# Kernel optimization log

Measured on AMD Instinct MI355X. Metric: run time of the kernel, lower is better.

The kernel has to match this reference:

```python
import jax, jax.numpy as jnp
import numpy as np

NUM_AUDIOS = 64
NODES_PER = 800
N = NUM_AUDIOS * NODES_PER  # 51200
DEG = 8
E = N * DEG  # 409600
IN_C, HID, OUT, HEADS = 512, 256, 256, 2
NEG_SLOPE = 0.2  # PyG GATConv default


def setup_inputs() -> dict:
    key = jax.random.key(0)
    ks = jax.random.split(key, 12)
    x = jax.random.normal(ks[0], (N, IN_C), jnp.float32)
    # edges strictly inside each audio's node block (PyG batching: no cross-graph edges)
    src_l = jax.random.randint(ks[1], (NUM_AUDIOS, NODES_PER * DEG), 0, NODES_PER)
    dst_l = jax.random.randint(ks[2], (NUM_AUDIOS, NODES_PER * DEG), 0, NODES_PER)
    off = (jnp.arange(NUM_AUDIOS) * NODES_PER)[:, None]
    edge_index = jnp.stack([(src_l + off).reshape(-1), (dst_l + off).reshape(-1)]).astype(jnp.int32)
    batch = jnp.repeat(jnp.arange(NUM_AUDIOS), NODES_PER).astype(jnp.int32)

    def gl(k, shape, fan):
        return (jax.random.normal(k, shape, jnp.float32) / np.sqrt(fan)).astype(jnp.float32)

    W1 = gl(ks[3], (IN_C, HEADS * HID), IN_C)
    a_s1 = gl(ks[4], (HEADS, HID), HID)
    a_d1 = gl(ks[5], (HEADS, HID), HID)
    b1 = jnp.zeros((HID,), jnp.float32)
    W2 = gl(ks[6], (HID, HEADS * OUT), HID)
    a_s2 = gl(ks[7], (HEADS, OUT), OUT)
    a_d2 = gl(ks[8], (HEADS, OUT), OUT)
    b2 = jnp.zeros((OUT,), jnp.float32)
    w_att = gl(ks[9], (OUT, 1), OUT)
    b_att = jnp.zeros((1,), jnp.float32)
    w_cls = gl(ks[10], (OUT, 2), OUT)
    b_cls = jnp.zeros((2,), jnp.float32)
    return dict(x=x, edge_index=edge_index, batch=batch,
                W1=W1, a_s1=a_s1, a_d1=a_d1, b1=b1,
                W2=W2, a_s2=a_s2, a_d2=a_d2, b2=b2,
                w_att=w_att, b_att=b_att, w_cls=w_cls, b_cls=b_cls)


def _gat(x, src, dst, W, a_s, a_d, b):
    """PyG GATConv(heads=H, concat=False): linear -> per-edge LeakyReLU scores ->
    softmax over incoming edges (with self-loops) -> scatter-sum -> head-mean + bias."""
    n = x.shape[0]
    H, C = a_s.shape
    h = (x @ W).reshape(n, H, C)                      # [N,H,C]
    al_s = jnp.einsum('nhc,hc->nh', h, a_s)           # [N,H]
    al_d = jnp.einsum('nhc,hc->nh', h, a_d)
    loop = jnp.arange(n, dtype=src.dtype)             # add self-loops (default)
    s = jnp.concatenate([src, loop])
    d = jnp.concatenate([dst, loop])
    e = jax.nn.leaky_relu(al_s[s] + al_d[d], NEG_SLOPE)  # [E+N,H]
    mx = jax.ops.segment_max(e, d, num_segments=n)
    w = jnp.exp(e - mx[d])
    den = jax.ops.segment_sum(w, d, num_segments=n)
    alpha = w / den[d]
    out = jax.ops.segment_sum(h[s] * alpha[:, :, None], d, num_segments=n)  # [N,H,C]
    return out.mean(axis=1) + b


def reference(x, edge_index, batch, W1, a_s1, a_d1, b1, W2, a_s2, a_d2, b2,
              w_att, b_att, w_cls, b_cls):
    src, dst = edge_index[0], edge_index[1]
    h = jax.nn.relu(_gat(x, src, dst, W1, a_s1, a_d1, b1))
    node_emb = _gat(h, src, dst, W2, a_s2, a_d2, b2)
    # per-audio temporal attention: softmax over nodes within each audio segment.
    # (edges never cross audio boundaries, so the per-subgraph GAT re-run in the
    #  original Python loop equals the full-graph GAT restricted to each segment.)
    logits = node_emb @ w_att + b_att                 # [N,1]
    mx = jax.ops.segment_max(logits, batch, num_segments=NUM_AUDIOS)
    w = jnp.exp(logits - mx[batch])
    den = jax.ops.segment_sum(w, batch, num_segments=NUM_AUDIOS)
    attn = w / den[batch]                             # [N,1]
    attended = jax.ops.segment_sum(attn * node_emb, batch, num_segments=NUM_AUDIOS)  # [A,OUT]
    audio_result = attended @ w_cls + b_cls           # [A,2]
    return node_emb, audio_result
```

## Files before the change

### kernel.cpp

```cpp
#include <hip/hip_runtime.h>
#include <cstdint>
#include <cstddef>

#define NUM_AUDIOS 64
#define NODES_PER  800
#define NN         51200
#define EE         409600

typedef __attribute__((ext_vector_type(8))) unsigned short ushort8;
typedef __attribute__((ext_vector_type(4))) unsigned short ushort4v;
typedef __attribute__((ext_vector_type(8))) __bf16 bf16x8;
typedef __attribute__((ext_vector_type(4))) float f32x4;

__device__ __forceinline__ float b2f(unsigned short h) {
  return __uint_as_float(((unsigned)h) << 16);
}
__device__ __forceinline__ unsigned short f2b(float f) {
  unsigned u = __float_as_uint(f);
  u += 0x7fffu + ((u >> 16) & 1u);
  return (unsigned short)(u >> 16);
}
__device__ __forceinline__ float lrelu(float v) { return v > 0.f ? v : 0.2f * v; }

#define P_AS1 0
#define P_AD1 512
#define P_B1  1024
#define P_AS2 1536
#define P_AD2 2048
#define P_B2  2560
#define P_WATT 3072
#define P_BATT 3328
#define P_WCLS 3336
#define P_BCLS 3848

#define ZERO_F4 132096
#define ZERO_BLOCKS 516

__global__ __launch_bounds__(256) void prolog0_k(float4* __restrict__ zbase,
                                                 const unsigned short* __restrict__ x,
                                                 int* __restrict__ flag) {
  const int i = blockIdx.x * 256 + threadIdx.x;
  if (i < ZERO_F4) zbase[i] = (float4){0.f, 0.f, 0.f, 0.f};
  if (blockIdx.x == 0) {
    __shared__ int s;
    if (threadIdx.x == 0) s = 0;
    __syncthreads();
    int big = 0;
    for (int k = threadIdx.x; k < 4096; k += 256) {
      const float v = b2f(x[k]);
      if (!(__builtin_fabsf(v) <= 1e4f)) big = 1;
    }
    if (big) atomicOr(&s, 1);
    __syncthreads();
    if (threadIdx.x == 0) *flag = s;
  }
}

#define PB_PAR  10
#define PB_T1   (PB_PAR + 1024)
#define PB_T2   (PB_T1 + 512)
#define PB_HIST (PB_T2 + 1600)

__global__ __launch_bounds__(256) void prep_k(
    const void* __restrict__ W1, unsigned short* __restrict__ W1T,
    const void* __restrict__ W2, unsigned short* __restrict__ W2T,
    const void* p0, const void* p1, const void* p2, const void* p3, const void* p4,
    const void* p5, const void* p6, const void* p7, const void* p8, const void* p9,
    unsigned short* __restrict__ params,
    const int* __restrict__ dst, int* __restrict__ counts,
    const int* __restrict__ flagp) {
  const int b = blockIdx.x, tid = threadIdx.x;
  const int f = *flagp;
  if (b < PB_PAR) {
    const void* srcs[10] = {p0, p1, p2, p3, p4, p5, p6, p7, p8, p9};
    const int offs[10] = {P_AS1, P_AD1, P_B1, P_AS2, P_AD2, P_B2, P_WATT, P_BATT, P_WCLS, P_BCLS};
    const int lens[10] = {512, 512, 256, 512, 512, 256, 256, 1, 512, 2};
    const int s = b;
    for (int i = tid; i < lens[s]; i += 256)
      params[offs[s] + i] = f ? f2b(((const float*)srcs[s])[i])
                              : ((const unsigned short*)srcs[s])[i];
  } else if (b < PB_T1) {
    const int idx = (b - PB_PAR) * 256 + tid;
    const int n = idx >> 9, k = idx & 511;
    W1T[idx] = f ? f2b(((const float*)W1)[(size_t)k * 512 + n])
                 : ((const unsigned short*)W1)[(size_t)k * 512 + n];
  } else if (b < PB_T2) {
    const int idx = (b - PB_T1) * 256 + tid;
    const int n = idx >> 8, k = idx & 255;
    W2T[idx] = f ? f2b(((const float*)W2)[(size_t)k * 512 + n])
                 : ((const unsigned short*)W2)[(size_t)k * 512 + n];
  } else {
    const int e = (b - PB_T2) * 256 + tid;
    atomicAdd(&counts[dst[e]], 1);
  }
}

__global__ __launch_bounds__(256) void rowptr_k(const int* __restrict__ counts, int* __restrict__ row_ptr) {
  __shared__ int sh[800];
  __shared__ int pre[200];
  const int a = blockIdx.x, t = threadIdx.x;
  for (int i = t; i < 800; i += 256) sh[i] = counts[a * 800 + i];
  __syncthreads();
  if (t < 200) pre[t] = sh[t * 4] + sh[t * 4 + 1] + sh[t * 4 + 2] + sh[t * 4 + 3];
  __syncthreads();
  if (t == 0) {
    int run = 0;
    for (int i = 0; i < 200; ++i) { const int v = pre[i]; pre[i] = run; run += v; }
  }
  __syncthreads();
  if (t < 200) {
    int b = a * 6400 + pre[t];
#pragma unroll
    for (int j = 0; j < 4; ++j) { row_ptr[a * 800 + t * 4 + j] = b; b += sh[t * 4 + j]; }
  }
}

__global__ __launch_bounds__(256) void scatter_k(const int* __restrict__ src, const int* __restrict__ dst,
                                                 const int* __restrict__ row_ptr, int* __restrict__ cursor,
                                                 int* __restrict__ ssrc) {
  const int e = blockIdx.x * 256 + threadIdx.x;
  const int d = dst[e];
  const int p = atomicAdd(&cursor[d], 1);
  ssrc[row_ptr[d] + p] = src[e];
}

__device__ __forceinline__ void mfma_tile(const unsigned short* As, const unsigned short* Bs,
                                          int wm, int wn, int row, int quad, f32x4 acc[4][4]) {
  bf16x8 af[4], bq[4];
  const int pa = (quad ^ (row & 3)) * 8;
#pragma unroll
  for (int i = 0; i < 4; ++i) {
    af[i] = *(const bf16x8*)&As[(wm * 64 + i * 16 + row) * 32 + pa];
    bq[i] = *(const bf16x8*)&Bs[(wn * 64 + i * 16 + row) * 32 + pa];
  }
#pragma unroll
  for (int i = 0; i < 4; ++i)
#pragma unroll
    for (int j = 0; j < 4; ++j)
      acc[i][j] = __builtin_amdgcn_mfma_f32_16x16x32_bf16(af[i], bq[j], acc[i][j], 0, 0, 0);
}

__global__ __launch_bounds__(256) void gemm_bt(const void* __restrict__ Araw,
                                               const unsigned short* __restrict__ BT,
                                               unsigned short* __restrict__ C,
                                               int K, int Nn,
                                               const unsigned short* __restrict__ a_s,
                                               const unsigned short* __restrict__ a_d,
                                               float* __restrict__ al_s,
                                               float* __restrict__ al_d,
                                               const int* __restrict__ aflag) {
  __shared__ unsigned short smem[16384];
  const int tid = threadIdx.x;
  const int wave = tid >> 6, lane = tid & 63;
  const int bid = blockIdx.x;
  const int g = bid & 7, bt = bid >> 3;
  const int m0 = (g * 50 + (bt >> 2)) * 128;
  const int n0 = (bt & 3) * 128;
  const int wm = wave >> 1, wn = wave & 1;
  const int row = lane & 15, quad = lane >> 4;
  f32x4 acc[4][4];
#pragma unroll
  for (int i = 0; i < 4; ++i)
#pragma unroll
    for (int j = 0; j < 4; ++j) acc[i][j] = (f32x4){0.f, 0.f, 0.f, 0.f};

  const bool a_is_f32 = (aflag != nullptr) && (*aflag != 0);
  const unsigned short* A16 = (const unsigned short*)Araw;
  const float* A32 = (const float*)Araw;
  const int srow0 = tid >> 2;
  const int kph = tid & 3;

  if (!a_is_f32) {
    const int nk = K >> 5;
    auto stage = [&](int buf, int k0) {
      unsigned short* Asb = smem + buf * 8192;
      unsigned short* Bsb = Asb + 4096;
#pragma unroll
      for (int r = 0; r < 2; ++r) {
        const int arow = r * 64 + srow0;
        const int kc = ((kph ^ (arow & 3)) * 8);
        __builtin_amdgcn_global_load_lds(
            (const __attribute__((address_space(1))) void*)(A16 + (size_t)(m0 + arow) * K + k0 + kc),
            (__attribute__((address_space(3))) void*)(Asb + (r * 256 + wave * 64) * 8),
            16, 0, 0);
        __builtin_amdgcn_global_load_lds(
            (const __attribute__((address_space(1))) void*)(BT + (size_t)(n0 + arow) * K + k0 + kc),
            (__attribute__((address_space(3))) void*)(Bsb + (r * 256 + wave * 64) * 8),
            16, 0, 0);
      }
    };
    stage(0, 0);
    for (int t = 0; t < nk; ++t) {
      const int cur = t & 1;
      if (t + 1 < nk) {
        stage(cur ^ 1, (t + 1) << 5);
        asm volatile("s_waitcnt vmcnt(4)" ::: "memory");
      } else {
        asm volatile("s_waitcnt vmcnt(0)" ::: "memory");
      }
      __builtin_amdgcn_sched_barrier(0);
      __builtin_amdgcn_s_barrier();
      __builtin_amdgcn_sched_barrier(0);
      mfma_tile(smem + cur * 8192, smem + cur * 8192 + 4096, wm, wn, row, quad, acc);
      __builtin_amdgcn_sched_barrier(0);
      __builtin_amdgcn_s_barrier();
    }
  } else {
    unsigned short* As = smem;
    unsigned short* Bs = smem + 4096;
    for (int k0 = 0; k0 < K; k0 += 32) {
      ushort8 pk[2];
#pragma unroll
      for (int r = 0; r < 2; ++r) {
        const int arow = r * 64 + srow0;
        const int kc = ((kph ^ (arow & 3)) * 8);
        const float* p = A32 + (size_t)(m0 + arow) * K + k0 + kc;
        const float4 f0 = *(const float4*)p;
        const float4 f1 = *(const float4*)(p + 4);
        pk[r][0] = f2b(f0.x); pk[r][1] = f2b(f0.y); pk[r][2] = f2b(f0.z); pk[r][3] = f2b(f0.w);
        pk[r][4] = f2b(f1.x); pk[r][5] = f2b(f1.y); pk[r][6] = f2b(f1.z); pk[r][7] = f2b(f1.w);
      }
      __syncthreads();
#pragma unroll
      for (int r = 0; r < 2; ++r) {
        const int arow = r * 64 + srow0;
        const int kc = ((kph ^ (arow & 3)) * 8);
        __builtin_amdgcn_global_load_lds(
            (const __attribute__((address_space(1))) void*)(BT + (size_t)(n0 + arow) * K + k0 + kc),
            (__attribute__((address_space(3))) void*)(Bs + (size_t)(r * 256 + wave * 64) * 8),
            16, 0, 0);
        *(ushort8*)&As[(size_t)(r * 256 + tid) * 8] = pk[r];
      }
      __syncthreads();
      mfma_tile(As, Bs, wm, wn, row, quad, acc);
    }
  }

  const int col = lane & 15;
  __syncthreads();
  {
#pragma unroll
    for (int i = 0; i < 4; ++i)
#pragma unroll
      for (int jj = 0; jj < 4; ++jj) {
#pragma unroll
        for (int r = 0; r < 4; ++r) {
          const int rl = wm * 64 + i * 16 + quad * 4 + r;
          const int pc = (wn * 4 + jj) ^ quad;
          smem[rl * 128 + pc * 16 + col] = f2b(acc[i][jj][r]);
        }
      }
  }
  __syncthreads();
  {
    const int rloc = tid >> 4;
    const int c8 = (tid & 15) * 8;
    const int lc = c8 >> 4;
    const int coff = c8 & 15;
#pragma unroll
    for (int s = 0; s < 8; ++s) {
      const int rl = s * 16 + rloc;
      const int q = (rl >> 2) & 3;
      const ushort8 v = *(const ushort8*)&smem[rl * 128 + (lc ^ q) * 16 + coff];
      *(ushort8*)&C[(size_t)(m0 + rl) * Nn + n0 + c8] = v;
    }
  }

  {
    const int head = (n0 + wn * 64) >> 8;
    float as4[4], ad4[4];
#pragma unroll
    for (int j = 0; j < 4; ++j) {
      const int gn = n0 + wn * 64 + j * 16 + col;
      as4[j] = b2f(a_s[gn]);
      ad4[j] = b2f(a_d[gn]);
    }
#pragma unroll
    for (int i = 0; i < 4; ++i)
#pragma unroll
      for (int r = 0; r < 4; ++r) {
        float ps = 0.f, pd = 0.f;
#pragma unroll
        for (int j = 0; j < 4; ++j) { ps += acc[i][j][r] * as4[j]; pd += acc[i][j][r] * ad4[j]; }
#pragma unroll
        for (int off = 1; off < 16; off <<= 1) {
          ps += __shfl_xor(ps, off);
          pd += __shfl_xor(pd, off);
        }
        if (col == 0) {
          const int gm = m0 + wm * 64 + i * 16 + quad * 4 + r;
          atomicAdd(&al_s[gm * 2 + head], ps);
          atomicAdd(&al_d[gm * 2 + head], pd);
        }
      }
  }
}

__global__ __launch_bounds__(256) void agg_k(const unsigned short* __restrict__ h,
                                             const float* __restrict__ al_s, const float* __restrict__ al_d,
                                             const int* __restrict__ row_ptr, const int* __restrict__ counts,
                                             const int* __restrict__ ssrc, const unsigned short* __restrict__ bias,
                                             unsigned short* __restrict__ out, int do_relu,
                                             void* __restrict__ out2, const int* __restrict__ flagp,
                                             const unsigned short* __restrict__ watt,
                                             float* __restrict__ lg) {
  const int wave = threadIdx.x >> 6, lane = threadIdx.x & 63;
  const int b = blockIdx.x;
  const int g = b & 7, r = b >> 3;
  const int a = g + 8 * (r / 200);
  const int chunk = r % 200;
  const int n = a * 800 + chunk * 4 + wave;
  const int head = lane >> 5;
  const int hl = lane & 31;
  const int hsel = lane & 32;
  const int deg = counts[n];
  const int base = row_ptr[n];
  const float ald = al_d[n * 2 + head];
  const float self_e = lrelu(al_s[n * 2 + head] + ald);

  float m = -1e30f;
  for (int i = hl; i < deg; i += 32) {
    const int s = ssrc[base + i];
    m = fmaxf(m, al_s[s * 2 + head]);
  }
#pragma unroll
  for (int off = 1; off < 32; off <<= 1) m = fmaxf(m, __shfl_xor(m, off));
  const float mx = fmaxf(lrelu(m + ald), self_e);

  const float w_self = __expf(self_e - mx);
  float acc[8];
  {
    const ushort8 hv = *(const ushort8*)&h[(unsigned)(n * 512 + lane * 8)];
#pragma unroll
    for (int j = 0; j < 8; ++j) acc[j] = w_self * b2f(hv[j]);
  }
  float dpart = 0.f;
  for (int t0 = 0; t0 < deg; t0 += 32) {
    const int cnt = min(32, deg - t0);
    int s = 0; float w = 0.f;
    if (hl < cnt) {
      s = ssrc[base + t0 + hl];
      w = __expf(lrelu(al_s[s * 2 + head] + ald) - mx);
      dpart += w;
    }
    for (int i = 0; i < cnt; ++i) {
      const float wb = __shfl(w, hsel + i);
      const int sb = __shfl(s, hsel + i);
      const ushort8 hv = *(const ushort8*)&h[(unsigned)(sb * 512 + lane * 8)];
#pragma unroll
      for (int j = 0; j < 8; ++j) acc[j] += wb * b2f(hv[j]);
    }
  }
#pragma unroll
  for (int off = 1; off < 32; off <<= 1) dpart += __shfl_xor(dpart, off);
  const float inv = 1.f / (w_self + dpart);

  const int c0 = hl * 8;
  ushort8 res;
  float ov[8];
#pragma unroll
  for (int j = 0; j < 8; ++j) {
    const float mine = acc[j] * inv;
    const float other = __shfl_xor(mine, 32);
    float o = (mine + other) * 0.5f + b2f(bias[c0 + j]);
    if (do_relu) o = fmaxf(o, 0.f);
    ov[j] = o;
    res[j] = f2b(o);
  }
  if (lane < 32) {
    *(ushort8*)&out[(unsigned)(n * 256 + c0)] = res;
    if (out2) {
      if (*flagp) {
        float4* p = (float4*)((float*)out2 + (size_t)n * 256 + c0);
        p[0] = (float4){ov[0], ov[1], ov[2], ov[3]};
        p[1] = (float4){ov[4], ov[5], ov[6], ov[7]};
      } else {
        *(ushort8*)((unsigned short*)out2 + (size_t)n * 256 + c0) = res;
      }
    }
    if (lg) {
      const ushort8 wv = *(const ushort8*)&watt[c0];
      float d = 0.f;
#pragma unroll
      for (int j = 0; j < 8; ++j) d += ov[j] * b2f(wv[j]);
#pragma unroll
      for (int off = 1; off < 32; off <<= 1) d += __shfl_xor(d, off);
      if (hl == 0) lg[n] = d + b2f(watt[256]);
    }
  }
}

__global__ __launch_bounds__(256) void stats_k(const float* __restrict__ lg,
                                               float* __restrict__ mxv, float* __restrict__ invv) {
  __shared__ float red[256];
  const int a = blockIdx.x, t = threadIdx.x;
  float m = -1e30f;
  for (int i = t; i < 800; i += 256) m = fmaxf(m, lg[a * 800 + i]);
  red[t] = m; __syncthreads();
  for (int s = 128; s >= 1; s >>= 1) { if (t < s) red[t] = fmaxf(red[t], red[t + s]); __syncthreads(); }
  const float mx = red[0];
  __syncthreads();
  float sum = 0.f;
  for (int i = t; i < 800; i += 256) sum += __expf(lg[a * 800 + i] - mx);
  red[t] = sum; __syncthreads();
  for (int s = 128; s >= 1; s >>= 1) { if (t < s) red[t] += red[t + s]; __syncthreads(); }
  if (t == 0) { mxv[a] = mx; invv[a] = 1.f / red[0]; }
}

__global__ __launch_bounds__(256) void attended_k(const unsigned short* __restrict__ emb,
                                                  const float* __restrict__ lg,
                                                  const float* __restrict__ mxv,
                                                  const float* __restrict__ invv,
                                                  float* __restrict__ attended) {
  const int b = blockIdx.x;
  const int a = b >> 3, chunk = b & 7;
  const int t = threadIdx.x;
  __shared__ float ws[100];
  const int i0 = chunk * 100;
  const float mx = mxv[a], inv = invv[a];
  if (t < 100) ws[t] = __expf(lg[a * 800 + i0 + t] - mx) * inv;
  __syncthreads();
  float acc = 0.f;
  const unsigned short* base = emb + ((size_t)(a * 800 + i0)) * 256 + t;
#pragma unroll 4
  for (int j = 0; j < 100; ++j) acc += ws[j] * b2f(base[(size_t)j * 256]);
  atomicAdd(&attended[a * 256 + t], acc);
}

__global__ __launch_bounds__(256) void cls_k(const float* __restrict__ attended,
                                             const unsigned short* __restrict__ params,
                                             void* __restrict__ out, const int* __restrict__ flag) {
  __shared__ float red[256];
  const int a = blockIdx.x, t = threadIdx.x;
  const float v = attended[a * 256 + t];
  const float p0 = v * b2f(params[P_WCLS + t * 2]);
  const float p1 = v * b2f(params[P_WCLS + t * 2 + 1]);
  red[t] = p0; __syncthreads();
  for (int s = 128; s >= 1; s >>= 1) { if (t < s) red[t] += red[t + s]; __syncthreads(); }
  const float r0 = red[0];
  __syncthreads();
  red[t] = p1; __syncthreads();
  for (int s = 128; s >= 1; s >>= 1) { if (t < s) red[t] += red[t + s]; __syncthreads(); }
  const float r1 = red[0];
  if (t == 0) {
    const float o0 = r0 + b2f(params[P_BCLS]);
    const float o1 = r1 + b2f(params[P_BCLS + 1]);
    if (*flag) {
      ((float*)out)[(size_t)NN * 256 + a * 2]     = o0;
      ((float*)out)[(size_t)NN * 256 + a * 2 + 1] = o1;
    } else {
      ((unsigned short*)out)[(size_t)NN * 256 + a * 2]     = f2b(o0);
      ((unsigned short*)out)[(size_t)NN * 256 + a * 2 + 1] = f2b(o1);
    }
  }
}

extern "C" void kernel_launch(void* const* d_in, const int* in_sizes, int n_in,
                              void* d_out, int out_size, void* d_ws, size_t ws_size,
                              hipStream_t stream) {
  (void)in_sizes; (void)n_in; (void)out_size; (void)ws_size;
  const void* x_raw  = d_in[0];
  const int*  eidx   = (const int*)d_in[1];
  const int* src = eidx;
  const int* dst = eidx + EE;

  char* ws = (char*)d_ws;
  size_t off = 0;
  auto alloc = [&](size_t bytes) -> void* {
    void* p = ws + off;
    off += (bytes + 255) & ~(size_t)255;
    return p;
  };
  int* flag              = (int*)alloc(256);
  unsigned short* params = (unsigned short*)alloc(4096 * 2);
  unsigned short* W1T    = (unsigned short*)alloc((size_t)512 * 512 * 2);
  unsigned short* W2T    = (unsigned short*)alloc((size_t)512 * 256 * 2);
  unsigned short* scr    = (unsigned short*)alloc((size_t)NN * 512 * 2);
  unsigned short* hbig   = (unsigned short*)alloc((size_t)NN * 512 * 2);
  int*   counts   = (int*)alloc((size_t)NN * 4);
  int*   cursor   = (int*)alloc((size_t)NN * 4);
  float* attended = (float*)alloc((size_t)NUM_AUDIOS * 256 * 4);
  float* al_s1    = (float*)alloc((size_t)NN * 2 * 4);
  float* al_d1    = (float*)alloc((size_t)NN * 2 * 4);
  float* al_s2    = (float*)alloc((size_t)NN * 2 * 4);
  float* al_d2    = (float*)alloc((size_t)NN * 2 * 4);
  int*   rowp   = (int*)alloc((size_t)NN * 4);
  int*   ssrc   = (int*)alloc((size_t)EE * 4);
  float* lg     = (float*)alloc((size_t)NN * 4);
  float* mxv    = (float*)alloc(NUM_AUDIOS * 4);
  float* invv   = (float*)alloc(NUM_AUDIOS * 4);
  unsigned short* hrel  = scr;
  unsigned short* emb16 = scr + (size_t)NN * 256;

  prolog0_k<<<dim3(ZERO_BLOCKS), 256, 0, stream>>>((float4*)counts,
                                                   (const unsigned short*)x_raw, flag);

  prep_k<<<dim3(PB_HIST), 256, 0, stream>>>(
      d_in[3], W1T, d_in[7], W2T,
      d_in[4], d_in[5], d_in[6], d_in[8], d_in[9],
      d_in[10], d_in[11], d_in[12], d_in[13], d_in[14],
      params, dst, counts, flag);

  rowptr_k<<<dim3(NUM_AUDIOS), 256, 0, stream>>>(counts, rowp);
  scatter_k<<<dim3(EE / 256), 256, 0, stream>>>(src, dst, rowp, cursor, ssrc);

  gemm_bt<<<dim3(1600), 256, 0, stream>>>(x_raw, W1T, hbig, 512, 512,
                                          params + P_AS1, params + P_AD1, al_s1, al_d1, flag);
  agg_k<<<dim3(NN / 4), 256, 0, stream>>>(hbig, al_s1, al_d1, rowp, counts, ssrc,
                                          params + P_B1, hrel, 1, nullptr, flag,
                                          params + P_WATT, nullptr);

  gemm_bt<<<dim3(1600), 256, 0, stream>>>(hrel, W2T, hbig, 256, 512,
                                          params + P_AS2, params + P_AD2, al_s2, al_d2, nullptr);
  agg_k<<<dim3(NN / 4), 256, 0, stream>>>(hbig, al_s2, al_d2, rowp, counts, ssrc,
                                          params + P_B2, emb16, 0, d_out, flag,
                                          params + P_WATT, lg);

  stats_k<<<dim3(NUM_AUDIOS), 256, 0, stream>>>(lg, mxv, invv);
  attended_k<<<dim3(NUM_AUDIOS * 8), 256, 0, stream>>>(emb16, lg, mxv, invv, attended);
  cls_k<<<dim3(NUM_AUDIOS), 256, 0, stream>>>(attended, params, d_out, flag);
}
```

Before: 449.2 us.

## Enlarge GEMM tile to 256x256 with 512 threads and reduce attention logits in LDS

The projection GEMM moves from 128x128 tiles with 256 threads to 256x256 tiles with 512 threads (8 waves, each 128x64), so each block covers a full head of columns. This raises operand reuse per LDS load and cuts the grid from 1600 to 400 blocks. The per-row attention logits are now summed across waves in shared memory and written with plain stores instead of global atomics, which works because one block owns a whole head. The tradeoff is more accumulator registers per thread, double the LDS use, fewer blocks to spread over the CUs, and an epilogue that writes the output in two halves.

```diff
diff --git a/kernel.cpp b/kernel.cpp
--- a/kernel.cpp
+++ b/kernel.cpp
@@ -8,7 +8,6 @@
 #define EE         409600
 
 typedef __attribute__((ext_vector_type(8))) unsigned short ushort8;
-typedef __attribute__((ext_vector_type(4))) unsigned short ushort4v;
 typedef __attribute__((ext_vector_type(8))) __bf16 bf16x8;
 typedef __attribute__((ext_vector_type(4))) float f32x4;
 
@@ -124,43 +123,46 @@
   ssrc[row_ptr[d] + p] = src[e];
 }
 
-__device__ __forceinline__ void mfma_tile(const unsigned short* As, const unsigned short* Bs,
-                                          int wm, int wn, int row, int quad, f32x4 acc[4][4]) {
-  bf16x8 af[4], bq[4];
+__device__ __forceinline__ void mfma_tile256(const unsigned short* As, const unsigned short* Bs,
+                                             int wm, int wn, int row, int quad, f32x4 acc[8][4]) {
+  bf16x8 af[8], bq[4];
   const int pa = (quad ^ (row & 3)) * 8;
 #pragma unroll
-  for (int i = 0; i < 4; ++i) {
-    af[i] = *(const bf16x8*)&As[(wm * 64 + i * 16 + row) * 32 + pa];
-    bq[i] = *(const bf16x8*)&Bs[(wn * 64 + i * 16 + row) * 32 + pa];
-  }
-#pragma unroll
-  for (int i = 0; i < 4; ++i)
+  for (int i = 0; i < 8; ++i)
+    af[i] = *(const bf16x8*)&As[(wm * 128 + i * 16 + row) * 32 + pa];
+#pragma unroll
+  for (int j = 0; j < 4; ++j)
+    bq[j] = *(const bf16x8*)&Bs[(wn * 64 + j * 16 + row) * 32 + pa];
+#pragma unroll
+  for (int i = 0; i < 8; ++i)
 #pragma unroll
     for (int j = 0; j < 4; ++j)
       acc[i][j] = __builtin_amdgcn_mfma_f32_16x16x32_bf16(af[i], bq[j], acc[i][j], 0, 0, 0);
 }
 
-__global__ __launch_bounds__(256) void gemm_bt(const void* __restrict__ Araw,
-                                               const unsigned short* __restrict__ BT,
-                                               unsigned short* __restrict__ C,
-                                               int K, int Nn,
-                                               const unsigned short* __restrict__ a_s,
-                                               const unsigned short* __restrict__ a_d,
-                                               float* __restrict__ al_s,
-                                               float* __restrict__ al_d,
-                                               const int* __restrict__ aflag) {
-  __shared__ unsigned short smem[16384];
+__global__ __launch_bounds__(512, 2) void gemm_bt(const void* __restrict__ Araw,
+                                                  const unsigned short* __restrict__ BT,
+                                                  unsigned short* __restrict__ C,
+                                                  int K, int Nn,
+                                                  const unsigned short* __restrict__ a_s,
+                                                  const unsigned short* __restrict__ a_d,
+                                                  float* __restrict__ al_s,
+                                                  float* __restrict__ al_d,
+                                                  const int* __restrict__ aflag) {
+  __shared__ unsigned short smem[32768];
   const int tid = threadIdx.x;
   const int wave = tid >> 6, lane = tid & 63;
   const int bid = blockIdx.x;
   const int g = bid & 7, bt = bid >> 3;
-  const int m0 = (g * 50 + (bt >> 2)) * 128;
-  const int n0 = (bt & 3) * 128;
-  const int wm = wave >> 1, wn = wave & 1;
+  const int mt = bt >> 1, nt = bt & 1;
+  const int m0 = (g * 25 + mt) * 256;
+  const int n0 = nt * 256;
+  const int wm = wave >> 2, wn = wave & 3;
   const int row = lane & 15, quad = lane >> 4;
-  f32x4 acc[4][4];
-#pragma unroll
-  for (int i = 0; i < 4; ++i)
+  const int col = lane & 15;
+  f32x4 acc[8][4];
+#pragma unroll
+  for (int i = 0; i < 8; ++i)
 #pragma unroll
     for (int j = 0; j < 4; ++j) acc[i][j] = (f32x4){0.f, 0.f, 0.f, 0.f};
 
@@ -173,19 +175,19 @@
   if (!a_is_f32) {
     const int nk = K >> 5;
     auto stage = [&](int buf, int k0) {
-      unsigned short* Asb = smem + buf * 8192;
-      unsigned short* Bsb = Asb + 4096;
-#pragma unroll
-      for (int r = 0; r < 2; ++r) {
-        const int arow = r * 64 + srow0;
+      unsigned short* Asb = smem + buf * 16384;
+      unsigned short* Bsb = Asb + 8192;
+#pragma unroll
+      for (int p = 0; p < 2; ++p) {
+        const int arow = p * 128 + srow0;
         const int kc = ((kph ^ (arow & 3)) * 8);
         __builtin_amdgcn_global_load_lds(
             (const __attribute__((address_space(1))) void*)(A16 + (size_t)(m0 + arow) * K + k0 + kc),
-            (__attribute__((address_space(3))) void*)(Asb + (r * 256 + wave * 64) * 8),
+            (__attribute__((address_space(3))) void*)(Asb + (p * 512 + tid) * 8),
             16, 0, 0);
         __builtin_amdgcn_global_load_lds(
             (const __attribute__((address_space(1))) void*)(BT + (size_t)(n0 + arow) * K + k0 + kc),
-            (__attribute__((address_space(3))) void*)(Bsb + (r * 256 + wave * 64) * 8),
+            (__attribute__((address_space(3))) void*)(Bsb + (p * 512 + tid) * 8),
             16, 0, 0);
       }
     };
@@ -201,73 +203,45 @@
       __builtin_amdgcn_sched_barrier(0);
       __builtin_amdgcn_s_barrier();
       __builtin_amdgcn_sched_barrier(0);
-      mfma_tile(smem + cur * 8192, smem + cur * 8192 + 4096, wm, wn, row, quad, acc);
+      mfma_tile256(smem + cur * 16384, smem + cur * 16384 + 8192, wm, wn, row, quad, acc);
       __builtin_amdgcn_sched_barrier(0);
       __builtin_amdgcn_s_barrier();
     }
   } else {
     unsigned short* As = smem;
-    unsigned short* Bs = smem + 4096;
+    unsigned short* Bs = smem + 8192;
     for (int k0 = 0; k0 < K; k0 += 32) {
       ushort8 pk[2];
 #pragma unroll
-      for (int r = 0; r < 2; ++r) {
-        const int arow = r * 64 + srow0;
+      for (int p = 0; p < 2; ++p) {
+        const int arow = p * 128 + srow0;
         const int kc = ((kph ^ (arow & 3)) * 8);
-        const float* p = A32 + (size_t)(m0 + arow) * K + k0 + kc;
-        const float4 f0 = *(const float4*)p;
-        const float4 f1 = *(const float4*)(p + 4);
-        pk[r][0] = f2b(f0.x); pk[r][1] = f2b(f0.y); pk[r][2] = f2b(f0.z); pk[r][3] = f2b(f0.w);
-        pk[r][4] = f2b(f1.x); pk[r][5] = f2b(f1.y); pk[r][6] = f2b(f1.z); pk[r][7] = f2b(f1.w);
+        const float* ap = A32 + (size_t)(m0 + arow) * K + k0 + kc;
+        const float4 f0 = *(const float4*)ap;
+        const float4 f1 = *(const float4*)(ap + 4);
+        pk[p][0] = f2b(f0.x); pk[p][1] = f2b(f0.y); pk[p][2] = f2b(f0.z); pk[p][3] = f2b(f0.w);
+        pk[p][4] = f2b(f1.x); pk[p][5] = f2b(f1.y); pk[p][6] = f2b(f1.z); pk[p][7] = f2b(f1.w);
       }
       __syncthreads();
 #pragma unroll
-      for (int r = 0; r < 2; ++r) {
-        const int arow = r * 64 + srow0;
+      for (int p = 0; p < 2; ++p) {
+        const int arow = p * 128 + srow0;
         const int kc = ((kph ^ (arow & 3)) * 8);
         __builtin_amdgcn_global_load_lds(
             (const __attribute__((address_space(1))) void*)(BT + (size_t)(n0 + arow) * K + k0 + kc),
-            (__attribute__((address_space(3))) void*)(Bs + (size_t)(r * 256 + wave * 64) * 8),
+            (__attribute__((address_space(3))) void*)(Bs + (size_t)(p * 512 + tid) * 8),
             16, 0, 0);
-        *(ushort8*)&As[(size_t)(r * 256 + tid) * 8] = pk[r];
+        *(ushort8*)&As[(size_t)(p * 512 + tid) * 8] = pk[p];
       }
       __syncthreads();
-      mfma_tile(As, Bs, wm, wn, row, quad, acc);
-    }
-  }
-
-  const int col = lane & 15;
-  __syncthreads();
+      mfma_tile256(As, Bs, wm, wn, row, quad, acc);
+    }
+  }
+
+  __syncthreads();
+
   {
-#pragma unroll
-    for (int i = 0; i < 4; ++i)
-#pragma unroll
-      for (int jj = 0; jj < 4; ++jj) {
-#pragma unroll
-        for (int r = 0; r < 4; ++r) {
-          const int rl = wm * 64 + i * 16 + quad * 4 + r;
-          const int pc = (wn * 4 + jj) ^ quad;
-          smem[rl * 128 + pc * 16 + col] = f2b(acc[i][jj][r]);
-        }
-      }
-  }
-  __syncthreads();
-  {
-    const int rloc = tid >> 4;
-    const int c8 = (tid & 15) * 8;
-    const int lc = c8 >> 4;
-    const int coff = c8 & 15;
-#pragma unroll
-    for (int s = 0; s < 8; ++s) {
-      const int rl = s * 16 + rloc;
-      const int q = (rl >> 2) & 3;
-      const ushort8 v = *(const ushort8*)&smem[rl * 128 + (lc ^ q) * 16 + coff];
-      *(ushort8*)&C[(size_t)(m0 + rl) * Nn + n0 + c8] = v;
-    }
-  }
-
-  {
-    const int head = (n0 + wn * 64) >> 8;
+    float* alb = (float*)smem;
     float as4[4], ad4[4];
 #pragma unroll
     for (int j = 0; j < 4; ++j) {
@@ -276,7 +250,7 @@
       ad4[j] = b2f(a_d[gn]);
     }
 #pragma unroll
-    for (int i = 0; i < 4; ++i)
+    for (int i = 0; i < 8; ++i)
 #pragma unroll
       for (int r = 0; r < 4; ++r) {
         float ps = 0.f, pd = 0.f;
@@ -288,11 +262,49 @@
           pd += __shfl_xor(pd, off);
         }
         if (col == 0) {
-          const int gm = m0 + wm * 64 + i * 16 + quad * 4 + r;
-          atomicAdd(&al_s[gm * 2 + head], ps);
-          atomicAdd(&al_d[gm * 2 + head], pd);
+          const int rr = wm * 128 + i * 16 + quad * 4 + r;
+          alb[(0 * 4 + wn) * 256 + rr] = ps;
+          alb[(1 * 4 + wn) * 256 + rr] = pd;
         }
       }
+  }
+  __syncthreads();
+  {
+    const float* alb = (const float*)smem;
+    const int rr = tid >> 1, kind = tid & 1;
+    float s = 0.f;
+#pragma unroll
+    for (int w = 0; w < 4; ++w) s += alb[(kind * 4 + w) * 256 + rr];
+    float* dstp = kind ? al_d : al_s;
+    dstp[(size_t)(m0 + rr) * 2 + nt] = s;
+  }
+  __syncthreads();
+
+#pragma unroll
+  for (int half = 0; half < 2; ++half) {
+    if (wm == half) {
+#pragma unroll
+      for (int i = 0; i < 8; ++i)
+#pragma unroll
+        for (int jj = 0; jj < 4; ++jj)
+#pragma unroll
+          for (int r = 0; r < 4; ++r) {
+            const int rl = i * 16 + quad * 4 + r;
+            const int pc = (wn * 4 + jj) ^ quad;
+            smem[rl * 256 + pc * 16 + col] = f2b(acc[i][jj][r]);
+          }
+    }
+    __syncthreads();
+#pragma unroll
+    for (int s = 0; s < 8; ++s) {
+      const int u = tid + 512 * s;
+      const int rw = u >> 5, unit = u & 31;
+      const int lc = unit >> 1, h16 = unit & 1;
+      const int q = (rw >> 2) & 3;
+      const ushort8 v = *(const ushort8*)&smem[rw * 256 + ((lc ^ q) * 16 + h16 * 8)];
+      *(ushort8*)&C[(size_t)(m0 + half * 128 + rw) * Nn + n0 + unit * 8] = v;
+    }
+    __syncthreads();
   }
 }
 
@@ -504,14 +516,14 @@
   rowptr_k<<<dim3(NUM_AUDIOS), 256, 0, stream>>>(counts, rowp);
   scatter_k<<<dim3(EE / 256), 256, 0, stream>>>(src, dst, rowp, cursor, ssrc);
 
-  gemm_bt<<<dim3(1600), 256, 0, stream>>>(x_raw, W1T, hbig, 512, 512,
-                                          params + P_AS1, params + P_AD1, al_s1, al_d1, flag);
+  gemm_bt<<<dim3(400), 512, 0, stream>>>(x_raw, W1T, hbig, 512, 512,
+                                         params + P_AS1, params + P_AD1, al_s1, al_d1, flag);
   agg_k<<<dim3(NN / 4), 256, 0, stream>>>(hbig, al_s1, al_d1, rowp, counts, ssrc,
                                           params + P_B1, hrel, 1, nullptr, flag,
                                           params + P_WATT, nullptr);
 
-  gemm_bt<<<dim3(1600), 256, 0, stream>>>(hrel, W2T, hbig, 256, 512,
-                                          params + P_AS2, params + P_AD2, al_s2, al_d2, nullptr);
+  gemm_bt<<<dim3(400), 512, 0, stream>>>(hrel, W2T, hbig, 256, 512,
+                                         params + P_AS2, params + P_AD2, al_s2, al_d2, nullptr);
   agg_k<<<dim3(NN / 4), 256, 0, stream>>>(hbig, al_s2, al_d2, rowp, counts, ssrc,
                                           params + P_B2, emb16, 0, d_out, flag,
                                           params + P_WATT, lg);
```

New measurement: 426.6 us. -5.0%, faster.
